# Optimization experiments

Hardware: AMD Instinct MI355X
Metric: run time of the kernel (lower is better)

The kernel has to match this reference:

```python
import jax, jax.numpy as jnp
import numpy as np
import math

C = 256
GROUPS = 8
EPS = 1e-5


def setup_inputs() -> dict:
    key = jax.random.key(0)
    ks = jax.random.split(key, 12)
    b, c, h, w = 4, C, 64, 64
    s = 1.0 / math.sqrt(c)
    return {
        "x": jax.random.normal(ks[0], (b, c, h, w), dtype=jnp.float32),
        "gamma": jax.random.normal(ks[1], (c,), dtype=jnp.float32) * 0.1 + 1.0,
        "beta": jax.random.normal(ks[2], (c,), dtype=jnp.float32) * 0.1,
        "wq": jax.random.normal(ks[3], (c, c), dtype=jnp.float32) * s,
        "bq": jnp.zeros((c,), dtype=jnp.float32),
        "wk": jax.random.normal(ks[4], (c, c), dtype=jnp.float32) * s,
        "bk": jnp.zeros((c,), dtype=jnp.float32),
        "wv": jax.random.normal(ks[5], (c, c), dtype=jnp.float32) * s,
        "bv": jnp.zeros((c,), dtype=jnp.float32),
        "wp": jax.random.normal(ks[6], (c, c), dtype=jnp.float32) * s,
        "bp": jnp.zeros((c,), dtype=jnp.float32),
    }


def _group_norm(x, gamma, beta):
    b, c, h, w = x.shape
    xg = x.reshape(b, GROUPS, c // GROUPS, h * w)
    mean = xg.mean(axis=(2, 3), keepdims=True)
    var = xg.var(axis=(2, 3), keepdims=True)
    xn = ((xg - mean) * jax.lax.rsqrt(var + EPS)).reshape(b, c, h, w)
    return xn * gamma[None, :, None, None] + beta[None, :, None, None]


def _conv1x1(x, w, b):
    # 1x1 conv == per-pixel channel GEMM
    return jnp.einsum('oc,bchw->bohw', w, x) + b[None, :, None, None]


def reference(x, gamma, beta, wq, bq, wk, bk, wv, bv, wp, bp):
    b, c, h, w = x.shape
    n = h * w
    xn = _group_norm(x, gamma, beta)
    q = _conv1x1(xn, wq, bq).reshape(b, c, n)  # [b,c,n]
    k = _conv1x1(xn, wk, bk).reshape(b, c, n)
    v = _conv1x1(xn, wv, bv).reshape(b, c, n)
    scale = 1.0 / math.sqrt(c)
    scores = jnp.einsum('bcn,bcm->bnm', q, k) * scale  # [b,n,n]
    attn = jax.nn.softmax(scores, axis=-1)
    out = jnp.einsum('bnm,bcm->bcn', attn, v).reshape(b, c, h, w)
    return _conv1x1(out, wp, bp) + x
```

## Files before the change

### kernel.cpp

```cpp
#include <hip/hip_runtime.h>
#include <hip/hip_bf16.h>
#include <math.h>


#define CCH 256
#define NPIX 4096
#define NB 4
#define NG 8
#define EPS 1e-5f
#define NCHUNK 4

typedef __attribute__((ext_vector_type(8))) short short8;
typedef __attribute__((ext_vector_type(4))) short short4v;
typedef __attribute__((ext_vector_type(4))) float f32x4;
typedef __attribute__((ext_vector_type(16))) float f32x16;
typedef unsigned short ushort_t;
typedef unsigned char u8;

#define GLD16(g, l) __builtin_amdgcn_global_load_lds( \
    (const __attribute__((address_space(1))) unsigned int*)(g), \
    (__attribute__((address_space(3))) unsigned int*)(l), 16, 0, 0)

__device__ inline ushort_t f2bf(float x) {
    union { float f; unsigned u; } c; c.f = x;
    unsigned r = c.u + 0x7FFFu + ((c.u >> 16) & 1u);
    return (ushort_t)(r >> 16);
}
__device__ inline float bf2f(ushort_t h) {
    union { unsigned u; float f; } c; c.u = ((unsigned)h) << 16;
    return c.f;
}
__device__ inline u8 f2fp8(float x) {
    return (u8)(__builtin_amdgcn_cvt_pk_fp8_f32(x, x, 0, false) & 0xff);
}
__device__ inline long mk64(unsigned lo, unsigned hi) {
    return (long)(((unsigned long long)hi << 32) | lo);
}

__global__ __launch_bounds__(256) void gn1w(const float* __restrict__ x,
                                            const float* __restrict__ wq,
                                            const float* __restrict__ wk,
                                            const float* __restrict__ wv,
                                            const float* __restrict__ wp,
                                            float* __restrict__ part,
                                            ushort_t* __restrict__ wbf,
                                            ushort_t* __restrict__ wpbf) {
    int bid = blockIdx.x;
    int t = threadIdx.x;
    if (bid >= 256) {
        int widx = bid - 256;
        int wi = widx >> 6;
        const float* src = wi == 0 ? wq : wi == 1 ? wk : wi == 2 ? wv : wp;
        ushort_t* dst = wi == 3 ? wpbf : wbf + wi * 65536;
        int i = (widx & 63) * 1024 + t * 4;
        float4 v = *(const float4*)(src + i);
        short4v o;
        o[0] = (short)f2bf(v.x); o[1] = (short)f2bf(v.y);
        o[2] = (short)f2bf(v.z); o[3] = (short)f2bf(v.w);
        *(short4v*)(dst + i) = o;
        return;
    }
    int bg = bid >> 3;
    int slice = bid & 7;
    const float* base = x + (size_t)bg * 32 * NPIX + (size_t)slice * 16384;
    float s = 0.f, sq = 0.f;
    for (int i = t; i < 4096; i += 256) {
        float4 v = ((const float4*)base)[i];
        s  += v.x + v.y + v.z + v.w;
        sq += v.x*v.x + v.y*v.y + v.z*v.z + v.w*v.w;
    }
    for (int off = 32; off; off >>= 1) {
        s  += __shfl_down(s,  off);
        sq += __shfl_down(sq, off);
    }
    __shared__ float red[8];
    int wid = t >> 6;
    if ((t & 63) == 0) { red[wid*2] = s; red[wid*2+1] = sq; }
    __syncthreads();
    if (t == 0) {
        float ts = 0.f, tq = 0.f;
        for (int wv2 = 0; wv2 < 4; wv2++) { ts += red[wv2*2]; tq += red[wv2*2+1]; }
        part[bid*2] = ts; part[bid*2+1] = tq;
    }
}

__global__ __launch_bounds__(256) void gn_transpose(const float* __restrict__ x,
                                                    const float* __restrict__ part,
                                                    const float* __restrict__ gamma,
                                                    const float* __restrict__ beta,
                                                    ushort_t* __restrict__ xnT) {
    __shared__ float T[64][69];
    __shared__ float gmean[2], grstd[2];
    int t = threadIdx.x;
    int nBase = blockIdx.x * 64;
    int cBase = blockIdx.y * 64;
    int b = blockIdx.z;
    if (t < 2) {
        int g = (cBase >> 5) + t;
        float s = 0.f, sq = 0.f;
        for (int i = 0; i < 8; i++) {
            s  += part[((b*NG + g)*8 + i)*2];
            sq += part[((b*NG + g)*8 + i)*2 + 1];
        }
        const float inv = 1.f / 131072.f;
        float mean = s * inv;
        float var = sq * inv - mean * mean;
        gmean[t] = mean;
        grstd[t] = rsqrtf(var + EPS);
    }
    __syncthreads();
    const float* xb = x + (size_t)b * CCH * NPIX;
    int n4  = (t & 15) * 4;
    int cc0 = (t >> 4) * 4;
    for (int i = 0; i < 4; i++) {
        int cc = cc0 + i;
        int c = cBase + cc;
        int gi = cc >> 5;
        float ga = gamma[c] * grstd[gi];
        float be = beta[c] - gmean[gi] * ga;
        float4 v = *(const float4*)&xb[(size_t)c * NPIX + nBase + n4];
        T[cc][n4+0] = v.x * ga + be;
        T[cc][n4+1] = v.y * ga + be;
        T[cc][n4+2] = v.z * ga + be;
        T[cc][n4+3] = v.w * ga + be;
    }
    __syncthreads();
    int nn  = t >> 2;
    int ci0 = (t & 3) * 16;
    short8 o0, o1;
    for (int j = 0; j < 8; j++) {
        o0[j] = (short)f2bf(T[ci0 + j][nn]);
        o1[j] = (short)f2bf(T[ci0 + 8 + j][nn]);
    }
    ushort_t* dst = xnT + ((size_t)b * NPIX + nBase + nn) * CCH + cBase + ci0;
    *(short8*)dst = o0;
    *((short8*)dst + 1) = o1;
}

__global__ __launch_bounds__(256, 2) void qkv3(const ushort_t* __restrict__ xnT,
                                               const ushort_t* __restrict__ wbf,
                                               const float* __restrict__ bq,
                                               const float* __restrict__ bk,
                                               const float* __restrict__ bv,
                                               u8* __restrict__ qT,
                                               u8* __restrict__ kT,
                                               u8* __restrict__ vv) {
    __shared__ __align__(16) ushort_t As[2][4096];
    __shared__ __align__(16) ushort_t Bs[2][4096];
    int t = threadIdx.x;
    int w = t >> 6, l = t & 63, quad = l >> 4, l16 = l & 15;
    int z = blockIdx.z;
    const ushort_t* A; const ushort_t* B; int mBase, nBase;
    if (z < 2) { A = xnT; B = wbf + z * 65536; mBase = blockIdx.x * 128; nBase = blockIdx.y * 128; }
    else       { A = wbf + 131072; B = xnT;    mBase = blockIdx.y * 128; nBase = blockIdx.x * 128; }
    int m0 = (w & 1) * 64, n0 = (w >> 1) * 64;

    const f32x4 fz = {0.f, 0.f, 0.f, 0.f};
    f32x4 acc[4][4];
    #pragma unroll
    for (int i = 0; i < 4; i++)
        #pragma unroll
        for (int j = 0; j < 4; j++) acc[i][j] = fz;

    int srow = t >> 2;
    int slc  = (t & 3) ^ ((t >> 2) & 3);
    int sldso = (t >> 6) * 512;

    #pragma unroll
    for (int j = 0; j < 2; j++) {
        int row = 64*j + srow;
        GLD16(A + (size_t)(mBase + row) * 256 + slc * 8, &As[0][j*2048 + sldso]);
        GLD16(B + (size_t)(nBase + row) * 256 + slc * 8, &Bs[0][j*2048 + sldso]);
    }
    int buf = 0;
    for (int kb = 0; kb < 8; kb++) {
        __syncthreads();
        if (kb < 7) {
            #pragma unroll
            for (int j = 0; j < 2; j++) {
                int row = 64*j + srow;
                GLD16(A + (size_t)(mBase + row) * 256 + (kb+1)*32 + slc * 8, &As[buf^1][j*2048 + sldso]);
                GLD16(B + (size_t)(nBase + row) * 256 + (kb+1)*32 + slc * 8, &Bs[buf^1][j*2048 + sldso]);
            }
        }
        short8 af[4], bfr[4];
        #pragma unroll
        for (int mb = 0; mb < 4; mb++)
            af[mb] = *(short8*)&As[buf][(m0 + mb*16 + l16)*32 + ((quad ^ (l16 & 3)) * 8)];
        #pragma unroll
        for (int nb = 0; nb < 4; nb++)
            bfr[nb] = *(short8*)&Bs[buf][(n0 + nb*16 + l16)*32 + ((quad ^ (l16 & 3)) * 8)];
        #pragma unroll
        for (int mb = 0; mb < 4; mb++)
            #pragma unroll
            for (int nb = 0; nb < 4; nb++)
                acc[mb][nb] = __builtin_amdgcn_mfma_f32_16x16x32_bf16(af[mb], bfr[nb], acc[mb][nb], 0, 0, 0);
        buf ^= 1;
    }
    if (z < 2) {
        const float* bias = z ? bk : bq;
        u8* C = z ? kT : qT;
        #pragma unroll
        for (int nb = 0; nb < 4; nb++) {
            int n = nBase + n0 + nb*16 + l16;
            float bb = bias[n];
            #pragma unroll
            for (int mb = 0; mb < 4; mb++)
                #pragma unroll
                for (int r = 0; r < 4; r++) {
                    int m = mBase + m0 + mb*16 + quad*4 + r;
                    C[(size_t)m * 256 + n] = f2fp8(acc[mb][nb][r] + bb);
                }
        }
    } else {
        #pragma unroll
        for (int mb = 0; mb < 4; mb++)
            #pragma unroll
            for (int r = 0; r < 4; r++) {
                int m = mBase + m0 + mb*16 + quad*4 + r;
                float bb = bv[m];
                #pragma unroll
                for (int nb = 0; nb < 4; nb++) {
                    int n = nBase + n0 + nb*16 + l16;
                    vv[((size_t)(n >> 12) * 256 + m) * 4096 + (n & 4095)] = f2fp8(acc[mb][nb][r] + bb);
                }
            }
    }
}

__global__ __launch_bounds__(128, 2) void flash_attn(const u8* __restrict__ qT,
                                                     const u8* __restrict__ kT,
                                                     const u8* __restrict__ vv,
                                                     ushort_t* __restrict__ Op0,
                                                     ushort_t* __restrict__ Op1,
                                                     ushort_t* __restrict__ Op2,
                                                     ushort_t* __restrict__ Op3,
                                                     float* __restrict__ lsum) {
    __shared__ __align__(16) u8 Ks[2][8192];
    __shared__ __align__(16) u8 Vs[3][8192];
    int t = threadIdx.x;
    int w = t >> 6, l = t & 63;
    int l32 = l & 31, hl = l >> 5;
    int flat = blockIdx.x + 64 * (blockIdx.y + 4 * blockIdx.z);
    int xcd = flat & 7;
    int ix = flat >> 3;
    int combo = xcd + 8 * (ix >> 6);
    int qt = ix & 63;
    int chunk = combo & 3, b = combo >> 2;
    int qBase = qt * 64;
    int qw = qBase + w * 32;

    long qf[16];
    {
        const u8* qrow = qT + ((size_t)b * NPIX + qw + l32) * 256 + hl * 8;
        #pragma unroll
        for (int cb = 0; cb < 16; cb++) qf[cb] = *(const long*)(qrow + cb * 16);
    }

    f32x16 accO[8];
    #pragma unroll
    for (int i = 0; i < 8; i++)
        #pragma unroll
        for (int r = 0; r < 16; r++) accO[i][r] = 0.f;
    float lqa = 0.f;

    const u8* kbase = kT + (size_t)b * NPIX * 256;
    const u8* vbase = vv + (size_t)b * 256 * NPIX;

    const float SC = 0.0625f * 1.44269504089f;
    int mStart = chunk * (NPIX / NCHUNK);
    const int NT = (NPIX / NCHUNK) / 32;

    int kkv[4], kcb[4], vc[4], vs[4];
    #pragma unroll
    for (int j = 0; j < 4; j++) {
        int n = j*128 + t;
        kkv[j] = n >> 4; kcb[j] = (n & 15) ^ (kkv[j] & 15);
        vc[j]  = n >> 1; vs[j]  = (n & 1) ^ ((vc[j] >> 2) & 1);
    }

    #pragma unroll
    for (int j = 0; j < 4; j++) {
        int n = j*128 + t;
        GLD16(kbase + (size_t)(mStart + kkv[j]) * 256 + kcb[j] * 16, &Ks[0][n*16]);
        GLD16(vbase + (size_t)vc[j] * NPIX + mStart + vs[j] * 16, &Vs[0][n*16]);
        GLD16(kbase + (size_t)(mStart + 32 + kkv[j]) * 256 + kcb[j] * 16, &Ks[1][n*16]);
        GLD16(vbase + (size_t)vc[j] * NPIX + mStart + 32 + vs[j] * 16, &Vs[1][n*16]);
    }
    __syncthreads();

    f32x16 sTa, sTb;
    #pragma unroll
    for (int r = 0; r < 16; r++) { sTa[r] = 0.f; sTb[r] = 0.f; }
    #pragma unroll
    for (int cb = 0; cb < 8; cb++) {
        long k0 = *(const long*)&Ks[0][(l32*16 + (cb ^ (l32 & 15)))*16 + hl*8];
        long k1 = *(const long*)&Ks[0][(l32*16 + ((cb+8) ^ (l32 & 15)))*16 + hl*8];
        sTa = __builtin_amdgcn_mfma_f32_32x32x16_fp8_fp8(k0, qf[cb],   sTa, 0, 0, 0);
        sTb = __builtin_amdgcn_mfma_f32_32x32x16_fp8_fp8(k1, qf[cb+8], sTb, 0, 0, 0);
    }

    int vcur = 0;
    for (int tt = 0; tt < NT; tt++) {
        float p[16];
        float part0 = 0.f, part1 = 0.f;
        #pragma unroll
        for (int r = 0; r < 16; r++) {
            float pe = exp2f(fmaf(sTa[r] + sTb[r], SC, -5.0f));
            pe = fminf(pe, 240.f);
            p[r] = pe;
            if (r & 1) part1 += pe; else part0 += pe;
        }
        lqa += part0 + part1;
        unsigned pkd[4];
        #pragma unroll
        for (int a = 0; a < 4; a++) {
            int u = __builtin_amdgcn_cvt_pk_fp8_f32(p[a*4+0], p[a*4+1], 0, false);
            u = __builtin_amdgcn_cvt_pk_fp8_f32(p[a*4+2], p[a*4+3], u, true);
            pkd[a] = (unsigned)u;
        }
        asm("v_permlane32_swap_b32 %0, %1" : "+v"(pkd[0]), "+v"(pkd[1]));
        asm("v_permlane32_swap_b32 %0, %1" : "+v"(pkd[2]), "+v"(pkd[3]));
        long B0 = mk64(pkd[0], pkd[1]);
        long B1 = mk64(pkd[2], pkd[3]);

        __syncthreads();
        if (tt + 2 < NT) {
            int m2 = mStart + (tt + 2) * 32;
            int vslot = vcur + 2; if (vslot >= 3) vslot -= 3;
            #pragma unroll
            for (int j = 0; j < 4; j++) {
                int n = j*128 + t;
                GLD16(kbase + (size_t)(m2 + kkv[j]) * 256 + kcb[j] * 16, &Ks[tt & 1][n*16]);
                GLD16(vbase + (size_t)vc[j] * NPIX + m2 + vs[j] * 16, &Vs[vslot][n*16]);
            }
        }

        __builtin_amdgcn_s_setprio(1);
        if (tt < NT - 1) {
            const u8* Kb = &Ks[(tt + 1) & 1][0];
            const u8* Vb = &Vs[vcur][0];
            #pragma unroll
            for (int r = 0; r < 16; r++) { sTa[r] = 0.f; sTb[r] = 0.f; }
            long v1d = 0;
            #pragma unroll
            for (int cb = 0; cb < 8; cb++) {
                long k0 = *(const long*)&Kb[(l32*16 + (cb ^ (l32 & 15)))*16 + hl*8];
                long k1 = *(const long*)&Kb[(l32*16 + ((cb+8) ^ (l32 & 15)))*16 + hl*8];
                int c = cb*32 + l32;
                int sw = (c >> 2) & 1;
                long v0 = *(const long*)&Vb[(c*2 + sw)*16 + hl*8];
                sTa = __builtin_amdgcn_mfma_f32_32x32x16_fp8_fp8(k0, qf[cb], sTa, 0, 0, 0);
                accO[cb] = __builtin_amdgcn_mfma_f32_32x32x16_fp8_fp8(v0, B0, accO[cb], 0, 0, 0);
                sTb = __builtin_amdgcn_mfma_f32_32x32x16_fp8_fp8(k1, qf[cb+8], sTb, 0, 0, 0);
                if (cb > 0)
                    accO[cb-1] = __builtin_amdgcn_mfma_f32_32x32x16_fp8_fp8(v1d, B1, accO[cb-1], 0, 0, 0);
                v1d = *(const long*)&Vb[(c*2 + (1 ^ sw))*16 + hl*8];
            }
            accO[7] = __builtin_amdgcn_mfma_f32_32x32x16_fp8_fp8(v1d, B1, accO[7], 0, 0, 0);
        } else {
            const u8* Vb = &Vs[vcur][0];
            #pragma unroll
            for (int cb = 0; cb < 8; cb++) {
                int c = cb*32 + l32;
                int sw = (c >> 2) & 1;
                long v0 = *(const long*)&Vb[(c*2 + sw)*16 + hl*8];
                accO[cb] = __builtin_amdgcn_mfma_f32_32x32x16_fp8_fp8(v0, B0, accO[cb], 0, 0, 0);
            }
            #pragma unroll
            for (int cb = 0; cb < 8; cb++) {
                int c = cb*32 + l32;
                int sw = (c >> 2) & 1;
                long v1 = *(const long*)&Vb[(c*2 + (1 ^ sw))*16 + hl*8];
                accO[cb] = __builtin_amdgcn_mfma_f32_32x32x16_fp8_fp8(v1, B1, accO[cb], 0, 0, 0);
            }
        }
        __builtin_amdgcn_s_setprio(0);
        vcur = vcur + 1; if (vcur >= 3) vcur = 0;
    }

    {
        float v = lqa + __shfl_xor(lqa, 32);
        if (hl == 0)
            lsum[((size_t)chunk * NB + b) * NPIX + qw + l32] = v;
    }
    ushort_t* op = chunk == 0 ? Op0 : chunk == 1 ? Op1 : chunk == 2 ? Op2 : Op3;
    size_t rowb = ((size_t)b * NPIX + qw + l32) * CCH;
    #pragma unroll
    for (int cblk = 0; cblk < 8; cblk++)
        #pragma unroll
        for (int a = 0; a < 4; a++) {
            short4v o;
            #pragma unroll
            for (int r = 0; r < 4; r++) o[r] = (short)f2bf(accO[cblk][a*4 + r]);
            *(short4v*)&op[rowb + cblk*32 + a*8 + hl*4] = o;
        }
}

__global__ __launch_bounds__(256) void attn_combine(ushort_t* __restrict__ Op0,
                                                    const ushort_t* __restrict__ Op1,
                                                    const ushort_t* __restrict__ Op2,
                                                    const ushort_t* __restrict__ Op3,
                                                    const float* __restrict__ lsum) {
    const size_t BN = (size_t)NB * NPIX;
    size_t base = ((size_t)blockIdx.x * 256 + threadIdx.x) * 4;
    size_t bn = base >> 8;
    float li = 1.f / (lsum[bn] + lsum[BN + bn] + lsum[2*BN + bn] + lsum[3*BN + bn]);
    short4v a0 = *(short4v*)&Op0[base];
    short4v a1 = *(const short4v*)&Op1[base];
    short4v a2 = *(const short4v*)&Op2[base];
    short4v a3 = *(const short4v*)&Op3[base];
    short4v o;
    #pragma unroll
    for (int i = 0; i < 4; i++) {
        float v = (bf2f((ushort_t)a0[i]) + bf2f((ushort_t)a1[i]) +
                   bf2f((ushort_t)a2[i]) + bf2f((ushort_t)a3[i])) * li;
        o[i] = (short)f2bf(v);
    }
    *(short4v*)&Op0[base] = o;
}

__global__ __launch_bounds__(256, 2) void projk(const ushort_t* __restrict__ wpbf,
                                                const ushort_t* __restrict__ aoT,
                                                const float* __restrict__ bp,
                                                const float* __restrict__ x,
                                                float* __restrict__ out) {
    __shared__ __align__(16) ushort_t As[2][4096];
    __shared__ __align__(16) ushort_t Bs[2][4096];
    int t = threadIdx.x;
    int w = t >> 6, l = t & 63, quad = l >> 4, l16 = l & 15;
    int mBase = blockIdx.y * 128, nBase = blockIdx.x * 128;
    int m0 = (w & 1) * 64, n0 = (w >> 1) * 64;

    const f32x4 fz = {0.f, 0.f, 0.f, 0.f};
    f32x4 acc[4][4];
    #pragma unroll
    for (int i = 0; i < 4; i++)
        #pragma unroll
        for (int j = 0; j < 4; j++) acc[i][j] = fz;

    int srow = t >> 2;
    int slc  = (t & 3) ^ ((t >> 2) & 3);
    int sldso = (t >> 6) * 512;

    #pragma unroll
    for (int j = 0; j < 2; j++) {
        int row = 64*j + srow;
        GLD16(wpbf + (size_t)(mBase + row) * 256 + slc * 8, &As[0][j*2048 + sldso]);
        GLD16(aoT  + (size_t)(nBase + row) * 256 + slc * 8, &Bs[0][j*2048 + sldso]);
    }
    int buf = 0;
    for (int kb = 0; kb < 8; kb++) {
        __syncthreads();
        if (kb < 7) {
            #pragma unroll
            for (int j = 0; j < 2; j++) {
                int row = 64*j + srow;
                GLD16(wpbf + (size_t)(mBase + row) * 256 + (kb+1)*32 + slc * 8, &As[buf^1][j*2048 + sldso]);
                GLD16(aoT  + (size_t)(nBase + row) * 256 + (kb+1)*32 + slc * 8, &Bs[buf^1][j*2048 + sldso]);
            }
        }
        short8 af[4], bfr[4];
        #pragma unroll
        for (int mb = 0; mb < 4; mb++)
            af[mb] = *(short8*)&As[buf][(m0 + mb*16 + l16)*32 + ((quad ^ (l16 & 3)) * 8)];
        #pragma unroll
        for (int nb = 0; nb < 4; nb++)
            bfr[nb] = *(short8*)&Bs[buf][(n0 + nb*16 + l16)*32 + ((quad ^ (l16 & 3)) * 8)];
        #pragma unroll
        for (int mb = 0; mb < 4; mb++)
            #pragma unroll
            for (int nb = 0; nb < 4; nb++)
                acc[mb][nb] = __builtin_amdgcn_mfma_f32_16x16x32_bf16(af[mb], bfr[nb], acc[mb][nb], 0, 0, 0);
        buf ^= 1;
    }
    #pragma unroll
    for (int mb = 0; mb < 4; mb++)
        #pragma unroll
        for (int r = 0; r < 4; r++) {
            int m = mBase + m0 + mb*16 + quad*4 + r;
            float bb = bp[m];
            #pragma unroll
            for (int nb = 0; nb < 4; nb++) {
                int n = nBase + n0 + nb*16 + l16;
                size_t idx = ((size_t)(n >> 12) * 256 + m) * 4096 + (n & 4095);
                out[idx] = acc[mb][nb][r] + bb + x[idx];
            }
        }
}

extern "C" void kernel_launch(void* const* d_in, const int* in_sizes, int n_in,
                              void* d_out, int out_size, void* d_ws, size_t ws_size,
                              hipStream_t stream) {
    const float* x     = (const float*)d_in[0];
    const float* gamma = (const float*)d_in[1];
    const float* beta  = (const float*)d_in[2];
    const float* wq    = (const float*)d_in[3];
    const float* bq    = (const float*)d_in[4];
    const float* wk    = (const float*)d_in[5];
    const float* bk    = (const float*)d_in[6];
    const float* wv    = (const float*)d_in[7];
    const float* bv    = (const float*)d_in[8];
    const float* wp    = (const float*)d_in[9];
    const float* bp    = (const float*)d_in[10];
    float* out = (float*)d_out;

    const size_t SZ = (size_t)NB * NPIX * CCH;
    float* part  = (float*)d_ws;
    float* lsum  = part + 512;
    ushort_t* wpbf = (ushort_t*)(lsum + (size_t)NCHUNK * NB * NPIX);
    ushort_t* slot0 = wpbf + 65536;
    ushort_t* Op3 = slot0;
    u8* qT8 = (u8*)(slot0 + SZ);
    u8* kT8 = (u8*)(slot0 + 2*SZ);
    u8* vv8 = (u8*)(slot0 + 3*SZ);
    ushort_t* aoT = slot0 + 4*SZ;
    ushort_t* xnT = (ushort_t*)d_out;
    ushort_t* Op1 = (ushort_t*)d_out;
    ushort_t* Op2 = (ushort_t*)d_out + SZ;
    ushort_t* wbf = (ushort_t*)d_out + SZ;

    gn1w<<<512, 256, 0, stream>>>(x, wq, wk, wv, wp, part, wbf, wpbf);
    gn_transpose<<<dim3(64, 4, 4), 256, 0, stream>>>(x, part, gamma, beta, xnT);
    qkv3<<<dim3(128, 2, 3), 256, 0, stream>>>(xnT, wbf, bq, bk, bv, qT8, kT8, vv8);
    flash_attn<<<dim3(64, NCHUNK, 4), 128, 0, stream>>>(qT8, kT8, vv8, aoT, Op1, Op2, Op3, lsum);
    attn_combine<<<(int)(SZ / 1024), 256, 0, stream>>>(aoT, Op1, Op2, Op3, lsum);
    projk<<<dim3(128, 2), 256, 0, stream>>>(wpbf, aoT, bp, x, out);
}
```

Before: 202.5 us.

## Use single-wave flash-attention blocks with vmcnt-based K/V pipelining instead of barriers

Each flash-attention block now holds a single 64-thread wave covering 32 queries, so twice as many blocks are launched. Because only one wave uses the shared K/V buffers, __syncthreads is replaced by explicit s_waitcnt vmcnt waits on the async global-to-LDS loads. V now uses double buffering instead of triple. The softmax pack moves to the end of each iteration, after the MFMAs, so it can overlap the next loads. The aim is to remove barrier stalls and overlap exp/pack work with the loads. The cost is that K/V tiles are no longer shared across two waves, which doubles LDS fill traffic per query.

```diff
diff --git a/kernel.cpp b/kernel.cpp
--- a/kernel.cpp
+++ b/kernel.cpp
@@ -20,6 +20,8 @@
 #define GLD16(g, l) __builtin_amdgcn_global_load_lds( \
     (const __attribute__((address_space(1))) unsigned int*)(g), \
     (__attribute__((address_space(3))) unsigned int*)(l), 16, 0, 0)
+
+#define WAITV(n) asm volatile("s_waitcnt vmcnt(" #n ")" ::: "memory")
 
 __device__ inline ushort_t f2bf(float x) {
     union { float f; unsigned u; } c; c.f = x;
@@ -228,27 +230,26 @@
     }
 }
 
-__global__ __launch_bounds__(128, 2) void flash_attn(const u8* __restrict__ qT,
-                                                     const u8* __restrict__ kT,
-                                                     const u8* __restrict__ vv,
-                                                     ushort_t* __restrict__ Op0,
-                                                     ushort_t* __restrict__ Op1,
-                                                     ushort_t* __restrict__ Op2,
-                                                     ushort_t* __restrict__ Op3,
-                                                     float* __restrict__ lsum) {
+__global__ __launch_bounds__(64, 2) void flash_attn(const u8* __restrict__ qT,
+                                                    const u8* __restrict__ kT,
+                                                    const u8* __restrict__ vv,
+                                                    ushort_t* __restrict__ Op0,
+                                                    ushort_t* __restrict__ Op1,
+                                                    ushort_t* __restrict__ Op2,
+                                                    ushort_t* __restrict__ Op3,
+                                                    float* __restrict__ lsum) {
     __shared__ __align__(16) u8 Ks[2][8192];
-    __shared__ __align__(16) u8 Vs[3][8192];
+    __shared__ __align__(16) u8 Vs[2][8192];
     int t = threadIdx.x;
-    int w = t >> 6, l = t & 63;
-    int l32 = l & 31, hl = l >> 5;
-    int flat = blockIdx.x + 64 * (blockIdx.y + 4 * blockIdx.z);
+    int l32 = t & 31, hl = t >> 5;
+    int t16 = t * 16;
+    int flat = blockIdx.x + 128 * (blockIdx.y + 4 * blockIdx.z);
     int xcd = flat & 7;
     int ix = flat >> 3;
-    int combo = xcd + 8 * (ix >> 6);
-    int qt = ix & 63;
+    int combo = xcd + 8 * (ix >> 7);
+    int qt = ix & 127;
     int chunk = combo & 3, b = combo >> 2;
-    int qBase = qt * 64;
-    int qw = qBase + w * 32;
+    int qw = qt * 32;
 
     long qf[16];
     {
@@ -271,23 +272,55 @@
     int mStart = chunk * (NPIX / NCHUNK);
     const int NT = (NPIX / NCHUNK) / 32;
 
-    int kkv[4], kcb[4], vc[4], vs[4];
-    #pragma unroll
-    for (int j = 0; j < 4; j++) {
-        int n = j*128 + t;
-        kkv[j] = n >> 4; kcb[j] = (n & 15) ^ (kkv[j] & 15);
-        vc[j]  = n >> 1; vs[j]  = (n & 1) ^ ((vc[j] >> 2) & 1);
-    }
-
-    #pragma unroll
-    for (int j = 0; j < 4; j++) {
-        int n = j*128 + t;
-        GLD16(kbase + (size_t)(mStart + kkv[j]) * 256 + kcb[j] * 16, &Ks[0][n*16]);
-        GLD16(vbase + (size_t)vc[j] * NPIX + mStart + vs[j] * 16, &Vs[0][n*16]);
-        GLD16(kbase + (size_t)(mStart + 32 + kkv[j]) * 256 + kcb[j] * 16, &Ks[1][n*16]);
-        GLD16(vbase + (size_t)vc[j] * NPIX + mStart + 32 + vs[j] * 16, &Vs[1][n*16]);
-    }
-    __syncthreads();
+    const u8* kaddr[8];
+    const u8* vaddr[8];
+    #pragma unroll
+    for (int j = 0; j < 8; j++) {
+        int n = j * 64 + t;
+        int kkv = n >> 4, kcb = (n & 15) ^ (kkv & 15);
+        int vc = n >> 1,  vsw = (n & 1) ^ ((vc >> 2) & 1);
+        kaddr[j] = kbase + (size_t)(mStart + kkv) * 256 + kcb * 16;
+        vaddr[j] = vbase + (size_t)vc * NPIX + mStart + vsw * 16;
+    }
+
+#define KISSUE(tile, kb_) { \
+        unsigned koff_ = (unsigned)(tile) * 8192u; \
+        _Pragma("unroll") \
+        for (int j = 0; j < 8; j++) \
+            GLD16(kaddr[j] + koff_, &Ks[kb_][j*1024 + t16]); }
+#define VISSUE(tile, vb_) { \
+        unsigned voff_ = (unsigned)(tile) * 32u; \
+        _Pragma("unroll") \
+        for (int j = 0; j < 8; j++) \
+            GLD16(vaddr[j] + voff_, &Vs[vb_][j*1024 + t16]); }
+
+#define SOFTMAX_PACK() { \
+        float p_[16]; float q0_ = 0.f, q1_ = 0.f; \
+        _Pragma("unroll") \
+        for (int r = 0; r < 16; r++) { \
+            float pe_ = exp2f(fmaf(sTa[r] + sTb[r], SC, -5.0f)); \
+            pe_ = fminf(pe_, 240.f); \
+            p_[r] = pe_; \
+            if (r & 1) q1_ += pe_; else q0_ += pe_; \
+        } \
+        lqa += q0_ + q1_; \
+        unsigned pk0_ = (unsigned)__builtin_amdgcn_cvt_pk_fp8_f32(p_[2], p_[3], \
+                        __builtin_amdgcn_cvt_pk_fp8_f32(p_[0], p_[1], 0, false), true); \
+        unsigned pk1_ = (unsigned)__builtin_amdgcn_cvt_pk_fp8_f32(p_[6], p_[7], \
+                        __builtin_amdgcn_cvt_pk_fp8_f32(p_[4], p_[5], 0, false), true); \
+        unsigned pk2_ = (unsigned)__builtin_amdgcn_cvt_pk_fp8_f32(p_[10], p_[11], \
+                        __builtin_amdgcn_cvt_pk_fp8_f32(p_[8], p_[9], 0, false), true); \
+        unsigned pk3_ = (unsigned)__builtin_amdgcn_cvt_pk_fp8_f32(p_[14], p_[15], \
+                        __builtin_amdgcn_cvt_pk_fp8_f32(p_[12], p_[13], 0, false), true); \
+        asm("v_permlane32_swap_b32 %0, %1" : "+v"(pk0_), "+v"(pk1_)); \
+        asm("v_permlane32_swap_b32 %0, %1" : "+v"(pk2_), "+v"(pk3_)); \
+        B0 = mk64(pk0_, pk1_); \
+        B1 = mk64(pk2_, pk3_); }
+
+    KISSUE(0, 0);
+    VISSUE(0, 0);
+    KISSUE(1, 1);
+    WAITV(16);
 
     f32x16 sTa, sTb;
     #pragma unroll
@@ -299,84 +332,59 @@
         sTa = __builtin_amdgcn_mfma_f32_32x32x16_fp8_fp8(k0, qf[cb],   sTa, 0, 0, 0);
         sTb = __builtin_amdgcn_mfma_f32_32x32x16_fp8_fp8(k1, qf[cb+8], sTb, 0, 0, 0);
     }
-
-    int vcur = 0;
-    for (int tt = 0; tt < NT; tt++) {
-        float p[16];
-        float part0 = 0.f, part1 = 0.f;
-        #pragma unroll
-        for (int r = 0; r < 16; r++) {
-            float pe = exp2f(fmaf(sTa[r] + sTb[r], SC, -5.0f));
-            pe = fminf(pe, 240.f);
-            p[r] = pe;
-            if (r & 1) part1 += pe; else part0 += pe;
-        }
-        lqa += part0 + part1;
-        unsigned pkd[4];
-        #pragma unroll
-        for (int a = 0; a < 4; a++) {
-            int u = __builtin_amdgcn_cvt_pk_fp8_f32(p[a*4+0], p[a*4+1], 0, false);
-            u = __builtin_amdgcn_cvt_pk_fp8_f32(p[a*4+2], p[a*4+3], u, true);
-            pkd[a] = (unsigned)u;
-        }
-        asm("v_permlane32_swap_b32 %0, %1" : "+v"(pkd[0]), "+v"(pkd[1]));
-        asm("v_permlane32_swap_b32 %0, %1" : "+v"(pkd[2]), "+v"(pkd[3]));
-        long B0 = mk64(pkd[0], pkd[1]);
-        long B1 = mk64(pkd[2], pkd[3]);
-
-        __syncthreads();
-        if (tt + 2 < NT) {
-            int m2 = mStart + (tt + 2) * 32;
-            int vslot = vcur + 2; if (vslot >= 3) vslot -= 3;
-            #pragma unroll
-            for (int j = 0; j < 4; j++) {
-                int n = j*128 + t;
-                GLD16(kbase + (size_t)(m2 + kkv[j]) * 256 + kcb[j] * 16, &Ks[tt & 1][n*16]);
-                GLD16(vbase + (size_t)vc[j] * NPIX + m2 + vs[j] * 16, &Vs[vslot][n*16]);
-            }
-        }
-
+    long B0, B1;
+    SOFTMAX_PACK();
+
+    #pragma unroll 1
+    for (int tt = 0; tt < NT - 1; ++tt) {
+        if (tt + 2 < NT) KISSUE(tt + 2, tt & 1);
+        VISSUE(tt + 1, (tt + 1) & 1);
+        if (tt + 2 < NT) { WAITV(16); } else { WAITV(8); }
+
+        const u8* Kb = &Ks[(tt + 1) & 1][0];
+        const u8* Vb = &Vs[tt & 1][0];
         __builtin_amdgcn_s_setprio(1);
-        if (tt < NT - 1) {
-            const u8* Kb = &Ks[(tt + 1) & 1][0];
-            const u8* Vb = &Vs[vcur][0];
-            #pragma unroll
-            for (int r = 0; r < 16; r++) { sTa[r] = 0.f; sTb[r] = 0.f; }
-            long v1d = 0;
-            #pragma unroll
-            for (int cb = 0; cb < 8; cb++) {
-                long k0 = *(const long*)&Kb[(l32*16 + (cb ^ (l32 & 15)))*16 + hl*8];
-                long k1 = *(const long*)&Kb[(l32*16 + ((cb+8) ^ (l32 & 15)))*16 + hl*8];
-                int c = cb*32 + l32;
-                int sw = (c >> 2) & 1;
-                long v0 = *(const long*)&Vb[(c*2 + sw)*16 + hl*8];
-                sTa = __builtin_amdgcn_mfma_f32_32x32x16_fp8_fp8(k0, qf[cb], sTa, 0, 0, 0);
-                accO[cb] = __builtin_amdgcn_mfma_f32_32x32x16_fp8_fp8(v0, B0, accO[cb], 0, 0, 0);
-                sTb = __builtin_amdgcn_mfma_f32_32x32x16_fp8_fp8(k1, qf[cb+8], sTb, 0, 0, 0);
-                if (cb > 0)
-                    accO[cb-1] = __builtin_amdgcn_mfma_f32_32x32x16_fp8_fp8(v1d, B1, accO[cb-1], 0, 0, 0);
-                v1d = *(const long*)&Vb[(c*2 + (1 ^ sw))*16 + hl*8];
-            }
-            accO[7] = __builtin_amdgcn_mfma_f32_32x32x16_fp8_fp8(v1d, B1, accO[7], 0, 0, 0);
-        } else {
-            const u8* Vb = &Vs[vcur][0];
-            #pragma unroll
-            for (int cb = 0; cb < 8; cb++) {
-                int c = cb*32 + l32;
-                int sw = (c >> 2) & 1;
-                long v0 = *(const long*)&Vb[(c*2 + sw)*16 + hl*8];
-                accO[cb] = __builtin_amdgcn_mfma_f32_32x32x16_fp8_fp8(v0, B0, accO[cb], 0, 0, 0);
-            }
-            #pragma unroll
-            for (int cb = 0; cb < 8; cb++) {
-                int c = cb*32 + l32;
-                int sw = (c >> 2) & 1;
-                long v1 = *(const long*)&Vb[(c*2 + (1 ^ sw))*16 + hl*8];
-                accO[cb] = __builtin_amdgcn_mfma_f32_32x32x16_fp8_fp8(v1, B1, accO[cb], 0, 0, 0);
-            }
-        }
+        #pragma unroll
+        for (int r = 0; r < 16; r++) { sTa[r] = 0.f; sTb[r] = 0.f; }
+        long v1d = 0;
+        #pragma unroll
+        for (int cb = 0; cb < 8; cb++) {
+            long k0 = *(const long*)&Kb[(l32*16 + (cb ^ (l32 & 15)))*16 + hl*8];
+            long k1 = *(const long*)&Kb[(l32*16 + ((cb+8) ^ (l32 & 15)))*16 + hl*8];
+            int c = cb*32 + l32;
+            int sw = (c >> 2) & 1;
+            long v0 = *(const long*)&Vb[(c*2 + sw)*16 + hl*8];
+            sTa = __builtin_amdgcn_mfma_f32_32x32x16_fp8_fp8(k0, qf[cb], sTa, 0, 0, 0);
+            accO[cb] = __builtin_amdgcn_mfma_f32_32x32x16_fp8_fp8(v0, B0, accO[cb], 0, 0, 0);
+            sTb = __builtin_amdgcn_mfma_f32_32x32x16_fp8_fp8(k1, qf[cb+8], sTb, 0, 0, 0);
+            if (cb > 0)
+                accO[cb-1] = __builtin_amdgcn_mfma_f32_32x32x16_fp8_fp8(v1d, B1, accO[cb-1], 0, 0, 0);
+            v1d = *(const long*)&Vb[(c*2 + (1 ^ sw))*16 + hl*8];
+        }
+        accO[7] = __builtin_amdgcn_mfma_f32_32x32x16_fp8_fp8(v1d, B1, accO[7], 0, 0, 0);
+        SOFTMAX_PACK();
         __builtin_amdgcn_s_setprio(0);
-        vcur = vcur + 1; if (vcur >= 3) vcur = 0;
+    }
+
+    WAITV(0);
+    {
+        const u8* Vb = &Vs[(NT - 1) & 1][0];
+        __builtin_amdgcn_s_setprio(1);
+        #pragma unroll
+        for (int cb = 0; cb < 8; cb++) {
+            int c = cb*32 + l32;
+            int sw = (c >> 2) & 1;
+            long v0 = *(const long*)&Vb[(c*2 + sw)*16 + hl*8];
+            accO[cb] = __builtin_amdgcn_mfma_f32_32x32x16_fp8_fp8(v0, B0, accO[cb], 0, 0, 0);
+        }
+        #pragma unroll
+        for (int cb = 0; cb < 8; cb++) {
+            int c = cb*32 + l32;
+            int sw = (c >> 2) & 1;
+            long v1 = *(const long*)&Vb[(c*2 + (1 ^ sw))*16 + hl*8];
+            accO[cb] = __builtin_amdgcn_mfma_f32_32x32x16_fp8_fp8(v1, B1, accO[cb], 0, 0, 0);
+        }
+        __builtin_amdgcn_s_setprio(0);
     }
 
     {
@@ -395,6 +403,9 @@
             for (int r = 0; r < 4; r++) o[r] = (short)f2bf(accO[cblk][a*4 + r]);
             *(short4v*)&op[rowb + cblk*32 + a*8 + hl*4] = o;
         }
+#undef KISSUE
+#undef VISSUE
+#undef SOFTMAX_PACK
 }
 
 __global__ __launch_bounds__(256) void attn_combine(ushort_t* __restrict__ Op0,
@@ -523,7 +534,7 @@
     gn1w<<<512, 256, 0, stream>>>(x, wq, wk, wv, wp, part, wbf, wpbf);
     gn_transpose<<<dim3(64, 4, 4), 256, 0, stream>>>(x, part, gamma, beta, xnT);
     qkv3<<<dim3(128, 2, 3), 256, 0, stream>>>(xnT, wbf, bq, bk, bv, qT8, kT8, vv8);
-    flash_attn<<<dim3(64, NCHUNK, 4), 128, 0, stream>>>(qT8, kT8, vv8, aoT, Op1, Op2, Op3, lsum);
+    flash_attn<<<dim3(128, NCHUNK, 4), 64, 0, stream>>>(qT8, kT8, vv8, aoT, Op1, Op2, Op3, lsum);
     attn_combine<<<(int)(SZ / 1024), 256, 0, stream>>>(aoT, Op1, Op2, Op3, lsum);
     projk<<<dim3(128, 2), 256, 0, stream>>>(wpbf, aoT, bp, x, out);
 }
```

Result: slower. 283.0 us (+39.8%).
